# Performance work log

Measured on AMD Instinct MI355X. Metric: run time of the kernel, lower is better.

## Reference

```python
import jax, jax.numpy as jnp
import numpy as np

P, Q, R, H1, H2, PH, B = 32, 32, 8, 128, 64, 16, 8192
PAIRS = P * Q
OUT = PAIRS * R  # X_Z_layer output units


def _pairwise_mask(p, q, r):
    # rows i*q+k correspond to pair (x_i, z_k): connected to x_i and z_k only
    mx = np.zeros((p * q, p), np.float32)
    for i in range(p):
        mx[i * q:(i + 1) * q, i] = 1.0
    mz = np.tile(np.eye(q, dtype=np.float32), (p, 1))
    m = np.concatenate([mx, mz], axis=1)          # [p*q, p+q]
    return np.repeat(m, r, axis=0)                 # [p*q*r, p+q]


def setup_inputs() -> dict:
    key = jax.random.key(0)
    ks = jax.random.split(key, 24)
    rn = lambda k, s, sc=0.1: jax.random.normal(k, s, jnp.float32) * sc
    x = jax.random.normal(ks[0], (B, P), jnp.float32)
    z = jax.random.normal(ks[1], (B, Q), jnp.float32)
    # X_mlp: P -> H1 -> H2 -> 1
    xw1, xb1 = rn(ks[2], (P, H1)), rn(ks[3], (H1,))
    xw2, xb2 = rn(ks[4], (H1, H2)), rn(ks[5], (H2,))
    xw3, xb3 = rn(ks[6], (H2, 1)), rn(ks[7], (1,))
    # Z_mlp: Q -> H1 -> H2 -> 1
    zw1, zb1 = rn(ks[8], (Q, H1)), rn(ks[9], (H1,))
    zw2, zb2 = rn(ks[10], (Q if False else H1, H2)), rn(ks[11], (H2,))
    zw3, zb3 = rn(ks[12], (H2, 1)), rn(ks[13], (1,))
    # masked X_Z_layer: weight pre-multiplied by structured mask (as in __init__)
    mask = jnp.asarray(_pairwise_mask(P, Q, R))    # [OUT, P+Q]
    xzw = (rn(ks[14], (OUT, P + Q)) * mask).T      # [P+Q, OUT]
    xzb = rn(ks[15], (OUT,))
    # 1024 tiny per-pair MLPs: R -> PH (bias) -> 1 (no bias), stacked
    pw1 = rn(ks[16], (PAIRS, R, PH))
    pb1 = rn(ks[17], (PAIRS, PH))
    pw2 = rn(ks[18], (PAIRS, PH))
    return dict(x=x, z=z, xw1=xw1, xb1=xb1, xw2=xw2, xb2=xb2, xw3=xw3, xb3=xb3,
                zw1=zw1, zb1=zb1, zw2=zw2, zb2=zb2, zw3=zw3, zb3=zb3,
                xzw=xzw, xzb=xzb, pw1=pw1, pb1=pb1, pw2=pw2)


def reference(x, z, xw1, xb1, xw2, xb2, xw3, xb3,
              zw1, zb1, zw2, zb2, zw3, zb3, xzw, xzb, pw1, pb1, pw2):
    relu = jax.nn.relu
    # main-effect MLPs
    hx = relu(relu(x @ xw1 + xb1) @ xw2 + xb2)
    out_x = hx @ xw3 + xb3                         # [B,1]
    hz = relu(relu(z @ zw1 + zb1) @ zw2 + zb2)
    out_z = hz @ zw3 + zb3                         # [B,1]
    # masked interaction layer
    xz = jnp.concatenate([x, z], axis=1)           # [B, P+Q]
    h = relu(xz @ xzw + xzb)                       # [B, OUT]
    # all 1024 per-pair MLPs as one batched GEMM
    hp = h.reshape(h.shape[0], PAIRS, R)           # [B, pairs, R]
    t = relu(jnp.einsum('bpr,prh->bph', hp, pw1) + pb1)
    out_xz = jnp.einsum('bph,ph->b', t, pw2)[:, None]  # sum over pairs -> [B,1]
    return out_x + out_z + out_xz
```

## Files before the change

kernel.cpp:

```cpp
#include <hip/hip_runtime.h>

#define B_TOT 8192
#define PP 32
#define QQ 32
#define RR 8
#define H1 128
#define H2 64
#define PHH 16
#define PAIRS 1024
#define OUT_UNITS 8192

#define NBLK_MM 512
#define NBLK_IA 4096

typedef float f32x16 __attribute__((ext_vector_type(16)));
typedef float f32x2  __attribute__((ext_vector_type(2)));
typedef short s16x8  __attribute__((ext_vector_type(8)));

union FragU { s16x8 v; unsigned int u[4]; };
union DU    { f32x16 v; f32x2 p[8]; };

__device__ inline unsigned int pack_bf16(float lo, float hi) {
    unsigned int r;
    asm("v_cvt_pk_bf16_f32 %0, %1, %2" : "=v"(r) : "v"(lo), "v"(hi));
    return r;
}

union SharedU {
    union {
        struct {
            float zT[16][128];
            float4 lwx[16][2];
            float4 lwz[16][2];
            float4 lhb[16][2];
            unsigned lpw1T[17][16][4];
            float lpbw[16][16][2];
        } s;
        float red[128][33];
    } ia;
    union {
        struct {
            union {
                float xT[32][36];
                float h1T[128][36];
            };
        };
        float red[32][68];
    } mm;
};

__global__ __launch_bounds__(256, 8) void fused_k(
    const float* __restrict__ x, const float* __restrict__ z,
    const float* __restrict__ xw1, const float* __restrict__ xb1,
    const float* __restrict__ xw2, const float* __restrict__ xb2,
    const float* __restrict__ xw3, const float* __restrict__ xb3,
    const float* __restrict__ zw1, const float* __restrict__ zb1,
    const float* __restrict__ zw2, const float* __restrict__ zb2,
    const float* __restrict__ zw3, const float* __restrict__ zb3,
    const float* __restrict__ xzw, const float* __restrict__ xzb,
    const float* __restrict__ pw1, const float* __restrict__ pb1,
    const float* __restrict__ pw2, float* __restrict__ out)
{
    __shared__ SharedU sh;
    const int bid  = blockIdx.x;
    const int t    = threadIdx.x;
    const int w    = t >> 6;
    const int lane = t & 63;
    const f32x2 zero2 = {0.f, 0.f};

    if (bid >= NBLK_MM) {
        const int ib    = bid - NBLK_MM;
        const int bx    = ib & 63;
        const int y     = ib >> 6;
        const int m     = lane & 31;
        const int kh    = lane >> 5;
        const int jj    = m & 15;
        const int cph   = m >> 4;
        const int b0    = bx * 128;
        const int i_x   = y >> 1;
        const int k0    = (y & 1) * 16;
        const int pair0 = y * 16;

        {
            int row = t >> 1;
            int c8  = (t & 1) * 8;
            const float* src = z + (size_t)(b0 + row) * 32 + k0 + c8;
            float4 a4 = *reinterpret_cast<const float4*>(src);
            float4 b4 = *reinterpret_cast<const float4*>(src + 4);
            sh.ia.s.zT[c8+0][row] = a4.x; sh.ia.s.zT[c8+1][row] = a4.y;
            sh.ia.s.zT[c8+2][row] = a4.z; sh.ia.s.zT[c8+3][row] = a4.w;
            sh.ia.s.zT[c8+4][row] = b4.x; sh.ia.s.zT[c8+5][row] = b4.y;
            sh.ia.s.zT[c8+6][row] = b4.z; sh.ia.s.zT[c8+7][row] = b4.w;
        }
        if (t < 128) {
            int p = t >> 3, c = t & 7;
            int gp = pair0 + p;
            reinterpret_cast<float*>(sh.ia.s.lwx)[t] = xzw[(size_t)i_x * OUT_UNITS + gp*8 + c];
            reinterpret_cast<float*>(sh.ia.s.lwz)[t] = xzw[(size_t)(32 + k0 + p) * OUT_UNITS + gp*8 + c];
            reinterpret_cast<float*>(sh.ia.s.lhb)[t] = xzb[gp*8 + c];
        }
        {
            int p = t >> 4, j = t & 15;
            int gp = pair0 + p;
            float2 bw;
            bw.x = pb1[gp*PHH + j];
            bw.y = pw2[gp*PHH + j];
            *reinterpret_cast<float2*>(sh.ia.s.lpbw[p][j]) = bw;
        }
        #pragma unroll
        for (int it = 0; it < 4; ++it) {
            int idx = t + it * 256;
            int p = idx >> 6, u = (idx >> 4) & 3, j = idx & 15;
            int gp = pair0 + p;
            float lo = pw1[(size_t)gp * 128 + (2*u)*16 + j];
            float hi = pw1[(size_t)gp * 128 + (2*u+1)*16 + j];
            sh.ia.s.lpw1T[p][j][u] = pack_bf16(lo, hi);
        }
        if (t < 64) reinterpret_cast<unsigned*>(sh.ia.s.lpw1T[16])[t] = 0u;

        const int bl = w * 32 + m;
        const float xv = x[(size_t)(b0 + bl) * 32 + i_x];
        __syncthreads();

        f32x2 acc2[8];
        #pragma unroll
        for (int r = 0; r < 8; ++r) acc2[r] = zero2;
        f32x16 zc;
        #pragma unroll
        for (int r = 0; r < 16; ++r) zc[r] = 0.f;

        const bool realB = (kh == cph);
        const f32x2 xvv = {xv, xv};

        #pragma unroll 2
        for (int ppl = 0; ppl < 8; ++ppl) {
            const int pAl = 2*ppl + kh;
            const int pBl = 2*ppl + cph;

            const float zv = sh.ia.s.zT[pAl][bl];
            const f32x2 zvv = {zv, zv};
            const f32x2* wx2 = reinterpret_cast<const f32x2*>(&sh.ia.s.lwx[pAl][0]);
            const f32x2* wz2 = reinterpret_cast<const f32x2*>(&sh.ia.s.lwz[pAl][0]);
            const f32x2* hb2 = reinterpret_cast<const f32x2*>(&sh.ia.s.lhb[pAl][0]);

            f32x2 h2[4];
            #pragma unroll
            for (int q = 0; q < 4; ++q) {
                f32x2 tt = __builtin_elementwise_fma(zvv, wz2[q], hb2[q]);
                tt = __builtin_elementwise_fma(xvv, wx2[q], tt);
                h2[q] = __builtin_elementwise_max(tt, zero2);
            }

            FragU a0, bf;
            a0.u[0] = pack_bf16(h2[0][0], h2[0][1]);
            a0.u[1] = pack_bf16(h2[1][0], h2[1][1]);
            a0.u[2] = pack_bf16(h2[2][0], h2[2][1]);
            a0.u[3] = pack_bf16(h2[3][0], h2[3][1]);

            const unsigned* bq = sh.ia.s.lpw1T[realB ? pBl : 16][jj];
            bf.u[0] = bq[0]; bf.u[1] = bq[1]; bf.u[2] = bq[2]; bf.u[3] = bq[3];

            const float2 bw = *reinterpret_cast<const float2*>(sh.ia.s.lpbw[pBl][jj]);
            const f32x2 bx2 = {bw.x, bw.x};
            const f32x2 by2 = {bw.y, bw.y};

            DU du;
            du.v = __builtin_amdgcn_mfma_f32_32x32x16_bf16(a0.v, bf.v, zc, 0, 0, 0);

            #pragma unroll
            for (int r = 0; r < 8; ++r) {
                f32x2 tt = __builtin_elementwise_max(du.p[r] + bx2, zero2);
                acc2[r] = __builtin_elementwise_fma(tt, by2, acc2[r]);
            }
        }

        __syncthreads();
        #pragma unroll
        for (int r = 0; r < 16; ++r) {
            int rowf = (r & 3) + 8 * (r >> 2) + 4 * kh;
            sh.ia.red[w * 32 + rowf][m] = acc2[r >> 1][r & 1];
        }
        __syncthreads();
        {
            int row = t >> 1, hh = t & 1;
            const float* rr = &sh.ia.red[row][hh * 16];
            float ssum = 0.f;
            #pragma unroll
            for (int c = 0; c < 16; ++c) ssum += rr[c];
            ssum += __shfl_xor(ssum, 1);
            if (hh == 0) atomicAdd(out + b0 + row, ssum);
        }
    } else {
        const int btile = bid & 255;
        const int which = bid >> 8;
        const float* in = which ? z   : x;
        const float* w1 = which ? zw1 : xw1;
        const float* b1 = which ? zb1 : xb1;
        const float* w2 = which ? zw2 : xw2;
        const float* b2 = which ? zb2 : xb2;
        const float* w3 = which ? zw3 : xw3;
        const float* b3 = which ? zb3 : xb3;
        const int b0 = btile * 32;
        const int bw = w * 8;

        {
            int row = t >> 3;
            int c4  = (t & 7) * 4;
            float4 v = *reinterpret_cast<const float4*>(in + (size_t)(b0 + row) * 32 + c4);
            sh.mm.xT[c4+0][row] = v.x; sh.mm.xT[c4+1][row] = v.y;
            sh.mm.xT[c4+2][row] = v.z; sh.mm.xT[c4+3][row] = v.w;
        }
        __syncthreads();

        const int j1 = lane, j2 = lane + 64;
        f32x2 a1p[4], a2p[4];
        {
            float bb1 = b1[j1], bb2 = b1[j2];
            f32x2 b1v = {bb1, bb1}, b2v = {bb2, bb2};
            #pragma unroll
            for (int i = 0; i < 4; ++i) { a1p[i] = b1v; a2p[i] = b2v; }
        }
        #pragma unroll 4
        for (int m = 0; m < 32; ++m) {
            const f32x2* xp = reinterpret_cast<const f32x2*>(&sh.mm.xT[m][bw]);
            float wv1 = w1[m*H1 + j1];
            float wv2 = w1[m*H1 + j2];
            f32x2 w1v = {wv1, wv1}, w2v = {wv2, wv2};
            #pragma unroll
            for (int q = 0; q < 4; ++q) {
                f32x2 xq = xp[q];
                a1p[q] = __builtin_elementwise_fma(xq, w1v, a1p[q]);
                a2p[q] = __builtin_elementwise_fma(xq, w2v, a2p[q]);
            }
        }
        __syncthreads();
        #pragma unroll
        for (int q = 0; q < 4; ++q) {
            f32x2 r1 = __builtin_elementwise_max(a1p[q], zero2);
            f32x2 r2 = __builtin_elementwise_max(a2p[q], zero2);
            sh.mm.h1T[j1][bw + 2*q + 0] = r1[0];
            sh.mm.h1T[j1][bw + 2*q + 1] = r1[1];
            sh.mm.h1T[j2][bw + 2*q + 0] = r2[0];
            sh.mm.h1T[j2][bw + 2*q + 1] = r2[1];
        }
        __syncthreads();

        f32x2 hp[4];
        {
            float b2v = b2[lane];
            f32x2 bb = {b2v, b2v};
            #pragma unroll
            for (int i = 0; i < 4; ++i) hp[i] = bb;
        }
        #pragma unroll 4
        for (int m = 0; m < 128; ++m) {
            float w2v = w2[m*H2 + lane];
            f32x2 wv = {w2v, w2v};
            const f32x2* hr = reinterpret_cast<const f32x2*>(&sh.mm.h1T[m][bw]);
            #pragma unroll
            for (int q = 0; q < 4; ++q)
                hp[q] = __builtin_elementwise_fma(hr[q], wv, hp[q]);
        }
        float hacc[8];
        {
            float w3v = w3[lane];
            #pragma unroll
            for (int q = 0; q < 4; ++q) {
                f32x2 r = __builtin_elementwise_max(hp[q], zero2);
                hacc[2*q+0] = r[0] * w3v;
                hacc[2*q+1] = r[1] * w3v;
            }
        }
        __syncthreads();
        #pragma unroll
        for (int i = 0; i < 8; ++i)
            sh.mm.red[bw + i][lane] = hacc[i];
        __syncthreads();
        if (t < 32) {
            float s = b3[0];
            const float4* rr = reinterpret_cast<const float4*>(&sh.mm.red[t][0]);
            #pragma unroll
            for (int c = 0; c < 16; ++c) {
                float4 v = rr[c];
                s += (v.x + v.y) + (v.z + v.w);
            }
            atomicAdd(out + b0 + t, s);
        }
    }
}

extern "C" void kernel_launch(void* const* d_in, const int* in_sizes, int n_in,
                              void* d_out, int out_size, void* d_ws, size_t ws_size,
                              hipStream_t stream) {
    const float* x   = (const float*)d_in[0];
    const float* z   = (const float*)d_in[1];
    const float* xw1 = (const float*)d_in[2];
    const float* xb1 = (const float*)d_in[3];
    const float* xw2 = (const float*)d_in[4];
    const float* xb2 = (const float*)d_in[5];
    const float* xw3 = (const float*)d_in[6];
    const float* xb3 = (const float*)d_in[7];
    const float* zw1 = (const float*)d_in[8];
    const float* zb1 = (const float*)d_in[9];
    const float* zw2 = (const float*)d_in[10];
    const float* zb2 = (const float*)d_in[11];
    const float* zw3 = (const float*)d_in[12];
    const float* zb3 = (const float*)d_in[13];
    const float* xzw = (const float*)d_in[14];
    const float* xzb = (const float*)d_in[15];
    const float* pw1 = (const float*)d_in[16];
    const float* pb1 = (const float*)d_in[17];
    const float* pw2 = (const float*)d_in[18];
    float* out = (float*)d_out;

    hipMemsetAsync(out, 0, (size_t)out_size * sizeof(float), stream);

    fused_k<<<dim3(NBLK_MM + NBLK_IA), 256, 0, stream>>>(
        x, z, xw1, xb1, xw2, xb2, xw3, xb3,
        zw1, zb1, zw2, zb2, zw3, zb3,
        xzw, xzb, pw1, pb1, pw2, out);
}
```

Baseline: 116.1 us.

## Process two x-indices per interaction block to reuse z tile

Each interaction block now handles 32 pairs (two adjacent x indices sharing the same z half), so the interaction grid is halved. The transposed z tile and the atomic output reduction are shared across twice the work, cutting redundant z loads and the number of atomics. In exchange, per-block LDS grows, the occupancy hint drops from 8 to 5 blocks per CU, and the inner loop is no longer unrolled.

Result: no change. 116.8 us (+0.6%).

```diff
diff --git a/kernel.cpp b/kernel.cpp
--- a/kernel.cpp
+++ b/kernel.cpp
@@ -11,7 +11,7 @@
 #define OUT_UNITS 8192
 
 #define NBLK_MM 512
-#define NBLK_IA 4096
+#define NBLK_IA 2048
 
 typedef float f32x16 __attribute__((ext_vector_type(16)));
 typedef float f32x2  __attribute__((ext_vector_type(2)));
@@ -30,11 +30,11 @@
     union {
         struct {
             float zT[16][128];
-            float4 lwx[16][2];
-            float4 lwz[16][2];
-            float4 lhb[16][2];
-            unsigned lpw1T[17][16][4];
-            float lpbw[16][16][2];
+            float4 lwx[32][2];
+            float4 lwz[32][2];
+            float4 lhb[32][2];
+            unsigned lpw1T[33][16][4];
+            float lpbw[32][16][2];
         } s;
         float red[128][33];
     } ia;
@@ -49,7 +49,7 @@
     } mm;
 };
 
-__global__ __launch_bounds__(256, 8) void fused_k(
+__global__ __launch_bounds__(256, 5) void fused_k(
     const float* __restrict__ x, const float* __restrict__ z,
     const float* __restrict__ xw1, const float* __restrict__ xb1,
     const float* __restrict__ xw2, const float* __restrict__ xb2,
@@ -71,15 +71,18 @@
     if (bid >= NBLK_MM) {
         const int ib    = bid - NBLK_MM;
         const int bx    = ib & 63;
-        const int y     = ib >> 6;
+        const int y2    = ib >> 6;
         const int m     = lane & 31;
         const int kh    = lane >> 5;
         const int jj    = m & 15;
         const int cph   = m >> 4;
         const int b0    = bx * 128;
-        const int i_x   = y >> 1;
-        const int k0    = (y & 1) * 16;
-        const int pair0 = y * 16;
+        const int par   = y2 & 1;
+        const int i_xb  = y2 & ~1;
+        const int k0    = par * 16;
+        const int oy0   = 2 * i_xb + par;
+        const int pair0_0 = oy0 * 16;
+        const int pair0_1 = (oy0 + 2) * 16;
 
         {
             int row = t >> 1;
@@ -92,34 +95,38 @@
             sh.ia.s.zT[c8+4][row] = b4.x; sh.ia.s.zT[c8+5][row] = b4.y;
             sh.ia.s.zT[c8+6][row] = b4.z; sh.ia.s.zT[c8+7][row] = b4.w;
         }
-        if (t < 128) {
-            int p = t >> 3, c = t & 7;
-            int gp = pair0 + p;
-            reinterpret_cast<float*>(sh.ia.s.lwx)[t] = xzw[(size_t)i_x * OUT_UNITS + gp*8 + c];
-            reinterpret_cast<float*>(sh.ia.s.lwz)[t] = xzw[(size_t)(32 + k0 + p) * OUT_UNITS + gp*8 + c];
-            reinterpret_cast<float*>(sh.ia.s.lhb)[t] = xzb[gp*8 + c];
-        }
-        {
-            int p = t >> 4, j = t & 15;
-            int gp = pair0 + p;
+        {
+            int pl = t >> 3, c = t & 7;
+            int sb = pl >> 4, p = pl & 15;
+            int gp = (sb ? pair0_1 : pair0_0) + p;
+            reinterpret_cast<float*>(sh.ia.s.lwx)[pl*8 + c] = xzw[(size_t)(i_xb + sb) * OUT_UNITS + gp*8 + c];
+            reinterpret_cast<float*>(sh.ia.s.lwz)[pl*8 + c] = xzw[(size_t)(32 + k0 + p) * OUT_UNITS + gp*8 + c];
+            reinterpret_cast<float*>(sh.ia.s.lhb)[pl*8 + c] = xzb[gp*8 + c];
+        }
+        #pragma unroll
+        for (int it = 0; it < 2; ++it) {
+            int idx = t + it * 256;
+            int p = idx >> 4, j = idx & 15;
+            int gp = ((p >> 4) ? pair0_1 : pair0_0) + (p & 15);
             float2 bw;
             bw.x = pb1[gp*PHH + j];
             bw.y = pw2[gp*PHH + j];
             *reinterpret_cast<float2*>(sh.ia.s.lpbw[p][j]) = bw;
         }
         #pragma unroll
-        for (int it = 0; it < 4; ++it) {
+        for (int it = 0; it < 8; ++it) {
             int idx = t + it * 256;
             int p = idx >> 6, u = (idx >> 4) & 3, j = idx & 15;
-            int gp = pair0 + p;
+            int gp = ((p >> 4) ? pair0_1 : pair0_0) + (p & 15);
             float lo = pw1[(size_t)gp * 128 + (2*u)*16 + j];
             float hi = pw1[(size_t)gp * 128 + (2*u+1)*16 + j];
             sh.ia.s.lpw1T[p][j][u] = pack_bf16(lo, hi);
         }
-        if (t < 64) reinterpret_cast<unsigned*>(sh.ia.s.lpw1T[16])[t] = 0u;
+        if (t < 64) reinterpret_cast<unsigned*>(sh.ia.s.lpw1T[32])[t] = 0u;
 
         const int bl = w * 32 + m;
-        const float xv = x[(size_t)(b0 + bl) * 32 + i_x];
+        const float2 xv2 = *reinterpret_cast<const float2*>(
+            x + (size_t)(b0 + bl) * 32 + i_xb);
         __syncthreads();
 
         f32x2 acc2[8];
@@ -130,47 +137,54 @@
         for (int r = 0; r < 16; ++r) zc[r] = 0.f;
 
         const bool realB = (kh == cph);
-        const f32x2 xvv = {xv, xv};
-
-        #pragma unroll 2
+
+        #pragma unroll 1
         for (int ppl = 0; ppl < 8; ++ppl) {
-            const int pAl = 2*ppl + kh;
-            const int pBl = 2*ppl + cph;
-
-            const float zv = sh.ia.s.zT[pAl][bl];
+            const int kA = 2*ppl + kh;
+            const int kB = 2*ppl + cph;
+            const float zv = sh.ia.s.zT[kA][bl];
             const f32x2 zvv = {zv, zv};
-            const f32x2* wx2 = reinterpret_cast<const f32x2*>(&sh.ia.s.lwx[pAl][0]);
-            const f32x2* wz2 = reinterpret_cast<const f32x2*>(&sh.ia.s.lwz[pAl][0]);
-            const f32x2* hb2 = reinterpret_cast<const f32x2*>(&sh.ia.s.lhb[pAl][0]);
-
-            f32x2 h2[4];
-            #pragma unroll
-            for (int q = 0; q < 4; ++q) {
-                f32x2 tt = __builtin_elementwise_fma(zvv, wz2[q], hb2[q]);
-                tt = __builtin_elementwise_fma(xvv, wx2[q], tt);
-                h2[q] = __builtin_elementwise_max(tt, zero2);
-            }
-
-            FragU a0, bf;
-            a0.u[0] = pack_bf16(h2[0][0], h2[0][1]);
-            a0.u[1] = pack_bf16(h2[1][0], h2[1][1]);
-            a0.u[2] = pack_bf16(h2[2][0], h2[2][1]);
-            a0.u[3] = pack_bf16(h2[3][0], h2[3][1]);
-
-            const unsigned* bq = sh.ia.s.lpw1T[realB ? pBl : 16][jj];
-            bf.u[0] = bq[0]; bf.u[1] = bq[1]; bf.u[2] = bq[2]; bf.u[3] = bq[3];
-
-            const float2 bw = *reinterpret_cast<const float2*>(sh.ia.s.lpbw[pBl][jj]);
-            const f32x2 bx2 = {bw.x, bw.x};
-            const f32x2 by2 = {bw.y, bw.y};
-
-            DU du;
-            du.v = __builtin_amdgcn_mfma_f32_32x32x16_bf16(a0.v, bf.v, zc, 0, 0, 0);
-
-            #pragma unroll
-            for (int r = 0; r < 8; ++r) {
-                f32x2 tt = __builtin_elementwise_max(du.p[r] + bx2, zero2);
-                acc2[r] = __builtin_elementwise_fma(tt, by2, acc2[r]);
+
+            #pragma unroll
+            for (int sb = 0; sb < 2; ++sb) {
+                const int pAl = sb*16 + kA;
+                const int pBl = sb*16 + kB;
+                const float xv = sb ? xv2.y : xv2.x;
+                const f32x2 xvv = {xv, xv};
+
+                const f32x2* wx2 = reinterpret_cast<const f32x2*>(&sh.ia.s.lwx[pAl][0]);
+                const f32x2* wz2 = reinterpret_cast<const f32x2*>(&sh.ia.s.lwz[pAl][0]);
+                const f32x2* hb2 = reinterpret_cast<const f32x2*>(&sh.ia.s.lhb[pAl][0]);
+
+                f32x2 h2[4];
+                #pragma unroll
+                for (int q = 0; q < 4; ++q) {
+                    f32x2 tt = __builtin_elementwise_fma(zvv, wz2[q], hb2[q]);
+                    tt = __builtin_elementwise_fma(xvv, wx2[q], tt);
+                    h2[q] = __builtin_elementwise_max(tt, zero2);
+                }
+
+                FragU a0, bf;
+                a0.u[0] = pack_bf16(h2[0][0], h2[0][1]);
+                a0.u[1] = pack_bf16(h2[1][0], h2[1][1]);
+                a0.u[2] = pack_bf16(h2[2][0], h2[2][1]);
+                a0.u[3] = pack_bf16(h2[3][0], h2[3][1]);
+
+                const unsigned* bq = sh.ia.s.lpw1T[realB ? pBl : 32][jj];
+                bf.u[0] = bq[0]; bf.u[1] = bq[1]; bf.u[2] = bq[2]; bf.u[3] = bq[3];
+
+                const float2 bw = *reinterpret_cast<const float2*>(sh.ia.s.lpbw[pBl][jj]);
+                const f32x2 bx2 = {bw.x, bw.x};
+                const f32x2 by2 = {bw.y, bw.y};
+
+                DU du;
+                du.v = __builtin_amdgcn_mfma_f32_32x32x16_bf16(a0.v, bf.v, zc, 0, 0, 0);
+
+                #pragma unroll
+                for (int r = 0; r < 8; ++r) {
+                    f32x2 tt = __builtin_elementwise_max(du.p[r] + bx2, zero2);
+                    acc2[r] = __builtin_elementwise_fma(tt, by2, acc2[r]);
+                }
             }
         }
 
```
